# Kernel optimization log

Hardware: AMD Instinct MI355X
Metric: run time of the kernel (lower is better)

The kernel has to match this reference:

```python
import jax, jax.numpy as jnp
import numpy as np

K = [3072, 1024, 512, 256, 128, 64, 32, 16, 8, 4, 2, 1]
R = 2          # Repeats
B = 8192       # batch
LEAK = 0.01    # LeakyReLU negative_slope
EP, EM, E0V = 50.0, -70.0, -65.0  # synapse reversal potentials


def setup_inputs() -> dict:
    key = jax.random.key(0)
    ks = jax.random.split(key, 40)
    std = float(np.sqrt(2.0 / K[0]))  # torch init: normal std sqrt(2/in_features)
    inp = {"x": jax.random.normal(ks[0], (B, K[0]), jnp.float32)}
    for j, name in enumerate(["ap1", "ap2", "am1", "am2", "g0"]):
        inp[name] = jax.random.normal(ks[1 + j], (R, K[0]), jnp.float32) * std
    for i in range(len(K) - 1):
        f = K[i] // K[i + 1]
        inp[f"w{i}"] = jax.random.normal(ks[6 + i], (R, K[i + 1], f), jnp.float32) * float(np.sqrt(1.0 / f))
        inp[f"b{i}"] = jnp.zeros((R, K[i + 1]), jnp.float32)  # bias.data.zero_()
    inp["root_w"] = jax.random.normal(ks[30], (1, R), jnp.float32) * 0.5
    inp["root_b"] = jnp.zeros((1,), jnp.float32)
    return inp


def _synapse(x, ap1, ap2, am1, am2, g0):
    # x: [B, N]; params: [R, N] -> out: [R, B, N]
    def g(a1, a2):
        return jnp.exp(jnp.clip(a1[:, None, :] * x[None, :, :] + a2[:, None, :], -60.0, 60.0))
    gp = g(ap1, ap2)
    gm = g(am1, am2)
    gz = g0[:, None, :]
    return (gp * EP + gm * EM + gz * E0V) / (gp + gm + gz)


def _tree(y, Ws, Bs):
    # y: [R, B, K0]; tree-structured (kronecker) linear layers + leaky relu
    for i in range(len(K) - 1):
        f = K[i] // K[i + 1]
        y = y.reshape(R, -1, K[i + 1], f)          # group fan-in children
        y = jnp.einsum('rbnf,rnf->rbn', y, Ws[i]) + Bs[i][:, None, :]
        y = jnp.where(y >= 0, y, LEAK * y)          # LeakyReLU(0.01)
    return y  # [R, B, 1]


def reference(x, ap1, ap2, am1, am2, g0,
              w0, w1, w2, w3, w4, w5, w6, w7, w8, w9, w10,
              b0, b1, b2, b3, b4, b5, b6, b7, b8, b9, b10,
              root_w, root_b):
    Ws = [w0, w1, w2, w3, w4, w5, w6, w7, w8, w9, w10]
    Bs = [b0, b1, b2, b3, b4, b5, b6, b7, b8, b9, b10]
    y = _synapse(x, ap1, ap2, am1, am2, g0)  # [R, B, 3072]
    y = _tree(y, Ws, Bs)                     # [R, B, 1]
    feats = y[:, :, 0].T                     # [B, R] (concat of repeat outputs)
    return feats @ root_w.T + root_b         # root linear -> [B, 1]
```

## Files before the change

### kernel.cpp

```cpp
#include <hip/hip_runtime.h>

#define K0 3072
#define BPB 32
#define BLOCK 1024

struct KtreeArgs {
  const float* x;
  const float* ap1; const float* ap2; const float* am1; const float* am2; const float* g0;
  const float* w[11];
  const float* bs[11];
  const float* root_w; const float* root_b;
  float* out;
};

__device__ __forceinline__ float lrelu(float v) {
  return v >= 0.0f ? v : 0.01f * v;
}

__device__ __forceinline__ int bitrev(int v, int bits) {
  int r = 0;
  for (int i = 0; i < bits; ++i) r |= ((v >> i) & 1) << (bits - 1 - i);
  return r;
}

__global__ __launch_bounds__(BLOCK, 4) void ktree_synapse_kernel(KtreeArgs A) {
  const int tid = threadIdx.x;
  const int wv  = tid >> 6;
  const int l   = tid & 63;
  const int c   = wv & 7;
  const int r   = wv >> 3;

  const int r6      = bitrev(l, 6);
  const int node512 = c * 64 + r6;
  const int kb      = node512 * 6;

  float p1[6], p2[6], m1[6], m2[6], z0[6];
  {
    const int o = r * K0 + kb;
    #pragma unroll
    for (int j = 0; j < 6; ++j) {
      p1[j] = A.ap1[o + j];
      p2[j] = A.ap2[o + j];
      m1[j] = A.am1[o + j];
      m2[j] = A.am2[o + j];
      z0[j] = A.g0[o + j];
    }
  }
  float w0v[6], b0a, b0b;
  {
    const int o = (r * 1024 + 2 * node512) * 3;
    #pragma unroll
    for (int j = 0; j < 6; ++j) w0v[j] = A.w[0][o + j];
    b0a = A.bs[0][r * 1024 + 2 * node512];
    b0b = A.bs[0][r * 1024 + 2 * node512 + 1];
  }
  float w1a, w1b, b1v;
  {
    const int n = r * 512 + node512;
    w1a = A.w[1][n * 2 + 0];
    w1b = A.w[1][n * 2 + 1];
    b1v = A.bs[1][n];
  }
  float ws0[6], ws1[6], bsv[6];
  #pragma unroll
  for (int s = 0; s < 6; ++s) {
    const int active = (l < (64 >> (s + 1)));
    const int local  = active ? bitrev(l, 5 - s) : 0;
    const int ktot   = 256 >> s;
    const int m      = r * ktot + c * (32 >> s) + local;
    ws0[s] = A.w[2 + s][m * 2 + 0];
    ws1[s] = A.w[2 + s][m * 2 + 1];
    bsv[s] = A.bs[2 + s][m];
  }

  __shared__ float lds_buf[BPB][2][8];

  const int bbase = blockIdx.x * BPB;
  const float LOG2E = 1.4426950408889634f;

  for (int bi = 0; bi < BPB; ++bi) {
    const int b = bbase + bi;
    const float2* xp = reinterpret_cast<const float2*>(A.x + (size_t)b * K0 + kb);
    const float2 xa = xp[0], xb = xp[1], xc = xp[2];
    const float xv[6] = {xa.x, xa.y, xb.x, xb.y, xc.x, xc.y};

    float acc0 = b0a, acc1 = b0b;
    #pragma unroll
    for (int j = 0; j < 6; ++j) {
      float tp = fmaf(p1[j], xv[j], p2[j]);
      float tm = fmaf(m1[j], xv[j], m2[j]);
      tp = fminf(fmaxf(tp, -60.0f), 60.0f);
      tm = fminf(fmaxf(tm, -60.0f), 60.0f);
      const float gp = __expf(tp);
      const float gm = __expf(tm);
      const float gz = z0[j];
      const float num = fmaf(50.0f, gp, fmaf(-70.0f, gm, -65.0f * gz));
      const float den = gp + gm + gz;
      float rr = __builtin_amdgcn_rcpf(den);
      rr = rr * fmaf(-den, rr, 2.0f);
      const float s = num * rr;
      if (j < 3) acc0 = fmaf(w0v[j], s, acc0);
      else       acc1 = fmaf(w0v[j], s, acc1);
    }
    acc0 = lrelu(acc0);
    acc1 = lrelu(acc1);
    float v = lrelu(fmaf(w1a, acc0, fmaf(w1b, acc1, b1v)));

    #pragma unroll
    for (int s = 0; s < 6; ++s) {
      const float u = __shfl_down(v, 32 >> s, 64);
      v = lrelu(fmaf(ws0[s], v, fmaf(ws1[s], u, bsv[s])));
    }
    if (l == 0) lds_buf[bi][r][c] = v;
  }
  __syncthreads();

  if (tid < BPB) {
    const int b = bbase + tid;
    float o = A.root_b[0];
    #pragma unroll
    for (int rr = 0; rr < 2; ++rr) {
      float v8[8];
      #pragma unroll
      for (int q = 0; q < 8; ++q) v8[q] = lds_buf[tid][rr][q];
      float v4[4];
      #pragma unroll
      for (int n = 0; n < 4; ++n)
        v4[n] = lrelu(fmaf(A.w[8][(rr * 4 + n) * 2 + 0], v8[2 * n],
                      fmaf(A.w[8][(rr * 4 + n) * 2 + 1], v8[2 * n + 1],
                           A.bs[8][rr * 4 + n])));
      float v2[2];
      #pragma unroll
      for (int n = 0; n < 2; ++n)
        v2[n] = lrelu(fmaf(A.w[9][(rr * 2 + n) * 2 + 0], v4[2 * n],
                      fmaf(A.w[9][(rr * 2 + n) * 2 + 1], v4[2 * n + 1],
                           A.bs[9][rr * 2 + n])));
      const float v1 = lrelu(fmaf(A.w[10][rr * 2 + 0], v2[0],
                             fmaf(A.w[10][rr * 2 + 1], v2[1],
                                  A.bs[10][rr])));
      o = fmaf(A.root_w[rr], v1, o);
    }
    A.out[b] = o;
  }
}

extern "C" void kernel_launch(void* const* d_in, const int* in_sizes, int n_in,
                              void* d_out, int out_size, void* d_ws, size_t ws_size,
                              hipStream_t stream) {
  KtreeArgs A;
  A.x   = (const float*)d_in[0];
  A.ap1 = (const float*)d_in[1];
  A.ap2 = (const float*)d_in[2];
  A.am1 = (const float*)d_in[3];
  A.am2 = (const float*)d_in[4];
  A.g0  = (const float*)d_in[5];
  for (int i = 0; i < 11; ++i) {
    A.w[i]  = (const float*)d_in[6 + 2 * i];
    A.bs[i] = (const float*)d_in[7 + 2 * i];
  }
  A.root_w = (const float*)d_in[28];
  A.root_b = (const float*)d_in[29];
  A.out = (float*)d_out;

  const int grid = 8192 / BPB;
  hipLaunchKernelGGL(ktree_synapse_kernel, dim3(grid), dim3(BLOCK), 0, stream, A);
}
```

Measured before the change: 216.4 us.

## Use butterfly xor shuffles, natural lane mapping, exp2 prescaling, and two-row batching

Replaces the bit-reversed lane mapping and shfl_down reduction with a natural node order and an xor-butterfly reduction. Each lane picks its own and partner weights by parity, so every lane computes a valid result at each level. The log2e factor is folded into the synapse parameters so exp becomes a raw exp2 with a scaled clamp, and -65*g0 is precomputed. Two batch rows are processed per iteration to expose more independent loads and shuffles, at the cost of extra registers under the 1024-thread launch bound.

```diff
diff --git a/kernel.cpp b/kernel.cpp
--- a/kernel.cpp
+++ b/kernel.cpp
@@ -3,6 +3,7 @@
 #define K0 3072
 #define BPB 32
 #define BLOCK 1024
+#define ROWS 2
 
 struct KtreeArgs {
   const float* x;
@@ -17,12 +18,6 @@
   return v >= 0.0f ? v : 0.01f * v;
 }
 
-__device__ __forceinline__ int bitrev(int v, int bits) {
-  int r = 0;
-  for (int i = 0; i < bits; ++i) r |= ((v >> i) & 1) << (bits - 1 - i);
-  return r;
-}
-
 __global__ __launch_bounds__(BLOCK, 4) void ktree_synapse_kernel(KtreeArgs A) {
   const int tid = threadIdx.x;
   const int wv  = tid >> 6;
@@ -30,20 +25,23 @@
   const int c   = wv & 7;
   const int r   = wv >> 3;
 
-  const int r6      = bitrev(l, 6);
-  const int node512 = c * 64 + r6;
+  const int node512 = c * 64 + l;
   const int kb      = node512 * 6;
 
-  float p1[6], p2[6], m1[6], m2[6], z0[6];
+  const float LOG2E = 1.4426950408889634f;
+  const float CL    = 60.0f * 1.4426950408889634f;
+
+  float p1l[6], p2l[6], m1l[6], m2l[6], z0v[6], z65[6];
   {
     const int o = r * K0 + kb;
     #pragma unroll
     for (int j = 0; j < 6; ++j) {
-      p1[j] = A.ap1[o + j];
-      p2[j] = A.ap2[o + j];
-      m1[j] = A.am1[o + j];
-      m2[j] = A.am2[o + j];
-      z0[j] = A.g0[o + j];
+      p1l[j] = A.ap1[o + j] * LOG2E;
+      p2l[j] = A.ap2[o + j] * LOG2E;
+      m1l[j] = A.am1[o + j] * LOG2E;
+      m2l[j] = A.am2[o + j] * LOG2E;
+      z0v[j] = A.g0[o + j];
+      z65[j] = -65.0f * z0v[j];
     }
   }
   float w0v[6], b0a, b0b;
@@ -61,57 +59,64 @@
     w1b = A.w[1][n * 2 + 1];
     b1v = A.bs[1][n];
   }
-  float ws0[6], ws1[6], bsv[6];
+  float wso[6], wst[6], bsv[6];
   #pragma unroll
   for (int s = 0; s < 6; ++s) {
-    const int active = (l < (64 >> (s + 1)));
-    const int local  = active ? bitrev(l, 5 - s) : 0;
-    const int ktot   = 256 >> s;
-    const int m      = r * ktot + c * (32 >> s) + local;
-    ws0[s] = A.w[2 + s][m * 2 + 0];
-    ws1[s] = A.w[2 + s][m * 2 + 1];
-    bsv[s] = A.bs[2 + s][m];
+    const int mo  = c * (32 >> s) + (l >> (s + 1));
+    const int idx = r * (256 >> s) + mo;
+    const int odd = (l >> s) & 1;
+    wso[s] = A.w[2 + s][idx * 2 + odd];
+    wst[s] = A.w[2 + s][idx * 2 + (odd ^ 1)];
+    bsv[s] = A.bs[2 + s][idx];
   }
 
   __shared__ float lds_buf[BPB][2][8];
+  const int bbase = blockIdx.x * BPB;
 
-  const int bbase = blockIdx.x * BPB;
-  const float LOG2E = 1.4426950408889634f;
+  for (int bi = 0; bi < BPB; bi += ROWS) {
+    float v[ROWS];
+    #pragma unroll
+    for (int u = 0; u < ROWS; ++u) {
+      const int b = bbase + bi + u;
+      const float2* xp = reinterpret_cast<const float2*>(A.x + (size_t)b * K0 + kb);
+      const float2 xa = xp[0], xb = xp[1], xc = xp[2];
+      const float xv[6] = {xa.x, xa.y, xb.x, xb.y, xc.x, xc.y};
 
-  for (int bi = 0; bi < BPB; ++bi) {
-    const int b = bbase + bi;
-    const float2* xp = reinterpret_cast<const float2*>(A.x + (size_t)b * K0 + kb);
-    const float2 xa = xp[0], xb = xp[1], xc = xp[2];
-    const float xv[6] = {xa.x, xa.y, xb.x, xb.y, xc.x, xc.y};
-
-    float acc0 = b0a, acc1 = b0b;
-    #pragma unroll
-    for (int j = 0; j < 6; ++j) {
-      float tp = fmaf(p1[j], xv[j], p2[j]);
-      float tm = fmaf(m1[j], xv[j], m2[j]);
-      tp = fminf(fmaxf(tp, -60.0f), 60.0f);
-      tm = fminf(fmaxf(tm, -60.0f), 60.0f);
-      const float gp = __expf(tp);
-      const float gm = __expf(tm);
-      const float gz = z0[j];
-      const float num = fmaf(50.0f, gp, fmaf(-70.0f, gm, -65.0f * gz));
-      const float den = gp + gm + gz;
-      float rr = __builtin_amdgcn_rcpf(den);
-      rr = rr * fmaf(-den, rr, 2.0f);
-      const float s = num * rr;
-      if (j < 3) acc0 = fmaf(w0v[j], s, acc0);
-      else       acc1 = fmaf(w0v[j], s, acc1);
+      float acc0 = b0a, acc1 = b0b;
+      #pragma unroll
+      for (int j = 0; j < 6; ++j) {
+        float tp = fmaf(p1l[j], xv[j], p2l[j]);
+        float tm = fmaf(m1l[j], xv[j], m2l[j]);
+        tp = fminf(fmaxf(tp, -CL), CL);
+        tm = fminf(fmaxf(tm, -CL), CL);
+        const float gp = __builtin_amdgcn_exp2f(tp);
+        const float gm = __builtin_amdgcn_exp2f(tm);
+        const float num = fmaf(50.0f, gp, fmaf(-70.0f, gm, z65[j]));
+        const float den = gp + gm + z0v[j];
+        float rr = __builtin_amdgcn_rcpf(den);
+        rr = rr * fmaf(-den, rr, 2.0f);
+        const float s = num * rr;
+        if (j < 3) acc0 = fmaf(w0v[j], s, acc0);
+        else       acc1 = fmaf(w0v[j], s, acc1);
+      }
+      acc0 = lrelu(acc0);
+      acc1 = lrelu(acc1);
+      v[u] = lrelu(fmaf(w1a, acc0, fmaf(w1b, acc1, b1v)));
     }
-    acc0 = lrelu(acc0);
-    acc1 = lrelu(acc1);
-    float v = lrelu(fmaf(w1a, acc0, fmaf(w1b, acc1, b1v)));
 
     #pragma unroll
     for (int s = 0; s < 6; ++s) {
-      const float u = __shfl_down(v, 32 >> s, 64);
-      v = lrelu(fmaf(ws0[s], v, fmaf(ws1[s], u, bsv[s])));
+      float pv[ROWS];
+      #pragma unroll
+      for (int u = 0; u < ROWS; ++u) pv[u] = __shfl_xor(v[u], 1 << s, 64);
+      #pragma unroll
+      for (int u = 0; u < ROWS; ++u)
+        v[u] = lrelu(fmaf(wso[s], v[u], fmaf(wst[s], pv[u], bsv[s])));
     }
-    if (l == 0) lds_buf[bi][r][c] = v;
+    if (l == 0) {
+      #pragma unroll
+      for (int u = 0; u < ROWS; ++u) lds_buf[bi + u][r][c] = v[u];
+    }
   }
   __syncthreads();
 
```

Result: slower. 248.7 us (+14.9%).
